# Optimization experiments

Hardware: AMD Instinct MI355X
Metric: run time of the kernel (lower is better)

Reference implementation:

```python
import jax, jax.numpy as jnp
import numpy as np

B, S, H, I = 2, 2048, 1024, 2816
NUM_EXPERTS = 8
NUM_SHARED = 1
E_ROUTED = NUM_EXPERTS - NUM_SHARED  # 7
TOP_K = 2


def setup_inputs() -> dict:
    key = jax.random.key(0)
    ks = jax.random.split(key, 9)
    scale = 0.02
    return {
        "x": jax.random.normal(ks[0], (B, S, H), jnp.float32),
        "router_w": jax.random.normal(ks[1], (H, E_ROUTED), jnp.float32) * scale,
        "routing_bias": jnp.zeros((E_ROUTED,), jnp.float32),
        "shared_gate": jax.random.normal(ks[2], (H, I), jnp.float32) * scale,
        "shared_up": jax.random.normal(ks[3], (H, I), jnp.float32) * scale,
        "shared_down": jax.random.normal(ks[4], (I, H), jnp.float32) * scale,
        "routed_gate": jax.random.normal(ks[5], (E_ROUTED, H, I), jnp.float32) * scale,
        "routed_up": jax.random.normal(ks[6], (E_ROUTED, H, I), jnp.float32) * scale,
        "routed_down": jax.random.normal(ks[7], (E_ROUTED, I, H), jnp.float32) * scale,
    }


def _mlp(x, gate_w, up_w, down_w):
    # SwiGLU MLP: down( silu(x@gate) * (x@up) )
    return (jax.nn.silu(x @ gate_w) * (x @ up_w)) @ down_w


def reference(x, router_w, routing_bias, shared_gate, shared_up, shared_down,
              routed_gate, routed_up, routed_down):
    e_routed = routed_gate.shape[0]
    # shared expert path (num_shared_experts == 1, no averaging)
    shared_out = _mlp(x, shared_gate, shared_up, shared_down)  # [B,S,H]

    # sigmoid router with bias, top-k, renormalize
    routing_logits = x @ router_w + routing_bias           # [B,S,E]
    routing_probs = jax.nn.sigmoid(routing_logits)
    scores, indices = jax.lax.top_k(routing_probs, TOP_K)  # [B,S,K]
    scores = scores / scores.sum(axis=-1, keepdims=True)

    # per-token combine weight for each expert: sum over top-k slots
    onehot = jax.nn.one_hot(indices, e_routed, dtype=x.dtype)   # [B,S,K,E]
    combine = jnp.einsum("bsk,bske->bse", scores, onehot)       # [B,S,E]

    out = shared_out
    for e in range(e_routed):  # fixed small expert count
        expert_out = _mlp(x, routed_gate[e], routed_up[e], routed_down[e])
        out = out + combine[..., e:e + 1] * expert_out
    return out
```

## Files before the change

### kernel.cpp

```cpp
#include <hip/hip_runtime.h>
#include <hip/hip_bf16.h>

#define TT 4096
#define HD 1024
#define ID 2816
#define ER 7
#define HI (HD * ID)

typedef short s16x8 __attribute__((ext_vector_type(8)));
typedef float f32x4 __attribute__((ext_vector_type(4)));

__device__ __forceinline__ uint32_t pkbf(float a, float b) {
    union { __hip_bfloat16 h[2]; uint32_t u; } z;
    z.h[0] = __float2bfloat16(a);
    z.h[1] = __float2bfloat16(b);
    return z.u;
}

__device__ __forceinline__ void gl_lds16(const void* g, void* l) {
    __builtin_amdgcn_global_load_lds(
        (const __attribute__((address_space(1))) uint32_t*)g,
        (__attribute__((address_space(3))) uint32_t*)l, 16, 0, 0);
}

__global__ __launch_bounds__(64) void router_kernel(
    const float* __restrict__ x, const float* __restrict__ rw,
    const float* __restrict__ rbias, float* __restrict__ combine)
{
    const int t = blockIdx.x;
    const int lane = threadIdx.x;
    const float* xt = x + (size_t)t * HD;
    float acc[ER];
#pragma unroll
    for (int e = 0; e < ER; ++e) acc[e] = 0.f;
    for (int h = lane; h < HD; h += 64) {
        const float xv = xt[h];
#pragma unroll
        for (int e = 0; e < ER; ++e)
            acc[e] += xv * rw[h * ER + e];
    }
#pragma unroll
    for (int e = 0; e < ER; ++e) {
        float v = acc[e];
#pragma unroll
        for (int off = 32; off > 0; off >>= 1) v += __shfl_down(v, off, 64);
        acc[e] = v;
    }
    if (lane == 0) {
        float p[ER];
#pragma unroll
        for (int e = 0; e < ER; ++e) {
            const float lg = acc[e] + rbias[e];
            p[e] = 1.f / (1.f + __expf(-lg));
        }
        int i1 = 0;
#pragma unroll
        for (int e = 1; e < ER; ++e) if (p[e] > p[i1]) i1 = e;
        int i2 = (i1 == 0) ? 1 : 0;
#pragma unroll
        for (int e = 0; e < ER; ++e) {
            if (e == i1 || e == i2) continue;
            if (p[e] > p[i2]) i2 = e;
        }
        const float s = p[i1] + p[i2];
        float w[8];
#pragma unroll
        for (int e = 0; e < 8; ++e) w[e] = 0.f;
        w[i1] = p[i1] / s;
        w[i2] = p[i2] / s;
        w[7] = 1.f;
        float* cb = combine + (size_t)t * 8;
#pragma unroll
        for (int e = 0; e < 8; ++e) cb[e] = w[e];
    }
}

__global__ __launch_bounds__(256) void txp_kernel(
    const float* __restrict__ Wsh, const float* __restrict__ Wrt,
    __hip_bfloat16* __restrict__ dst, int K, int N)
{
    __shared__ float lds[64 * 65];
    const int z = blockIdx.z;
    const float* src = (z < ER) ? (Wrt + (size_t)z * HI) : Wsh;
    __hip_bfloat16* out = dst + (size_t)z * HI;
    const int n0 = blockIdx.x * 64, k0 = blockIdx.y * 64;
    const int t = threadIdx.x;
    const int r = t >> 4, c = (t & 15) * 4;
#pragma unroll
    for (int i = 0; i < 4; ++i) {
        const float4 v = *(const float4*)(src + (size_t)(k0 + r + 16 * i) * N + n0 + c);
        float* p = &lds[(r + 16 * i) * 65 + c];
        p[0] = v.x; p[1] = v.y; p[2] = v.z; p[3] = v.w;
    }
    __syncthreads();
    const int nr = t >> 3, kc = (t & 7) * 8;
#pragma unroll
    for (int i = 0; i < 2; ++i) {
        const int nn = nr + 32 * i;
        uint32_t w[4];
#pragma unroll
        for (int j = 0; j < 4; ++j)
            w[j] = pkbf(lds[(kc + 2 * j) * 65 + nn], lds[(kc + 2 * j + 1) * 65 + nn]);
        *(uint4*)(out + (size_t)(n0 + nn) * K + k0 + kc) = *(uint4*)w;
    }
}

__global__ __launch_bounds__(256) void cvt_kernel(
    const float* __restrict__ a, __hip_bfloat16* __restrict__ o)
{
    const size_t i = ((size_t)blockIdx.x * 256 + threadIdx.x) * 8;
    const float4 v0 = *(const float4*)(a + i);
    const float4 v1 = *(const float4*)(a + i + 4);
    uint32_t w[4] = { pkbf(v0.x, v0.y), pkbf(v0.z, v0.w),
                      pkbf(v1.x, v1.y), pkbf(v1.z, v1.w) };
    *(uint4*)(o + i) = *(uint4*)w;
}

__global__ __launch_bounds__(256) void zero_kernel(float* __restrict__ o)
{
    const size_t i = ((size_t)blockIdx.x * 256 + threadIdx.x) * 4;
    *(float4*)(o + i) = float4{0.f, 0.f, 0.f, 0.f};
}

__global__ __launch_bounds__(256) void gu_kernel_g(
    const __hip_bfloat16* __restrict__ X,
    const __hip_bfloat16* __restrict__ Wg,
    const __hip_bfloat16* __restrict__ Wu,
    const float* __restrict__ combine,
    __hip_bfloat16* __restrict__ H,
    int e0)
{
    __shared__ __hip_bfloat16 sA[128 * 32];
    __shared__ __hip_bfloat16 sG[128 * 32];
    __shared__ __hip_bfloat16 sU[128 * 32];
    const int tid = threadIdx.x;
    const int g = gridDim.z;

    const int lid = blockIdx.x + 22 * blockIdx.y + 704 * blockIdx.z;
    const int xcd = lid & 7;
    const int w = lid >> 3;
    const int xpe = 8 / g;
    const int el = xcd / xpe;
    const int t = xcd % xpe;
    const int cx = (xpe >= 2) ? 2 : 1;
    const int tw = 22 / cx;
    const int th = 32 / (xpe / cx);
    const int bx = (t % cx) * tw + (w % tw);
    const int by = (t / cx) * th + (w / tw);

    const int e = e0 + el;
    const int n0 = bx * 128, m0 = by * 128;
    const __hip_bfloat16* Bg = Wg + (size_t)e * HI;
    const __hip_bfloat16* Bu = Wu + (size_t)e * HI;
    const int ldH = g * ID;

    const int lane = tid & 63, wave = tid >> 6;
    const int wm = (wave >> 1) * 64, wn = (wave & 1) * 64;
    const int r = lane & 15, quad = lane >> 4;

    f32x4 ag[4][4], au[4][4];
#pragma unroll
    for (int i = 0; i < 4; ++i)
#pragma unroll
        for (int j = 0; j < 4; ++j) {
            ag[i][j] = (f32x4){0.f, 0.f, 0.f, 0.f};
            au[i][j] = (f32x4){0.f, 0.f, 0.f, 0.f};
        }

    const int srow = tid >> 2;
    const int sk = ((tid & 3) ^ ((srow >> 1) & 3)) * 8;
    const size_t aoff = (size_t)(m0 + srow) * HD + sk;
    const size_t boff = (size_t)(n0 + srow) * HD + sk;
    char* lA = (char*)sA + tid * 16;
    char* lG = (char*)sG + tid * 16;
    char* lU = (char*)sU + tid * 16;

    const int xh = ((quad ^ ((r >> 1) & 3)) << 4);

    for (int kb = 0; kb < HD; kb += 32) {
        gl_lds16(X + aoff + kb, lA);
        gl_lds16(X + aoff + (size_t)64 * HD + kb, lA + 4096);
        gl_lds16(Bg + boff + kb, lG);
        gl_lds16(Bg + boff + (size_t)64 * HD + kb, lG + 4096);
        gl_lds16(Bu + boff + kb, lU);
        gl_lds16(Bu + boff + (size_t)64 * HD + kb, lU + 4096);
        __syncthreads();

        s16x8 af[4], bg[4], bu[4];
#pragma unroll
        for (int mi = 0; mi < 4; ++mi)
            af[mi] = *(const s16x8*)((const char*)sA + (wm + mi * 16 + r) * 64 + xh);
#pragma unroll
        for (int ni = 0; ni < 4; ++ni) {
            bg[ni] = *(const s16x8*)((const char*)sG + (wn + ni * 16 + r) * 64 + xh);
            bu[ni] = *(const s16x8*)((const char*)sU + (wn + ni * 16 + r) * 64 + xh);
        }
#pragma unroll
        for (int mi = 0; mi < 4; ++mi)
#pragma unroll
            for (int ni = 0; ni < 4; ++ni) {
                ag[mi][ni] = __builtin_amdgcn_mfma_f32_16x16x32_bf16(af[mi], bg[ni], ag[mi][ni], 0, 0, 0);
                au[mi][ni] = __builtin_amdgcn_mfma_f32_16x16x32_bf16(af[mi], bu[ni], au[mi][ni], 0, 0, 0);
            }
        __syncthreads();
    }

    const int colb = el * ID;
#pragma unroll
    for (int mi = 0; mi < 4; ++mi)
#pragma unroll
        for (int i = 0; i < 4; ++i) {
            const int grow = m0 + wm + mi * 16 + quad * 4 + i;
            const float wcb = combine[(size_t)grow * 8 + e];
#pragma unroll
            for (int ni = 0; ni < 4; ++ni) {
                const int gcol = n0 + wn + ni * 16 + r;
                const float gv = ag[mi][ni][i];
                const float uv = au[mi][ni][i];
                const float hv = (gv / (1.f + __expf(-gv))) * uv * wcb;
                H[(size_t)grow * ldH + colb + gcol] = __float2bfloat16(hv);
            }
        }
}

__global__ __launch_bounds__(256) void down_kernel_g(
    const __hip_bfloat16* __restrict__ Hb,
    const __hip_bfloat16* __restrict__ Wd,
    float* __restrict__ Out, int g)
{
    __shared__ __hip_bfloat16 sA[128 * 32];
    __shared__ __hip_bfloat16 sB[128 * 32];
    const int tid = threadIdx.x;

    const int lid = blockIdx.x + 8 * blockIdx.y + 256 * blockIdx.z;
    const int xcd = lid & 7;
    const int w = lid >> 3;
    const int sz = xcd >> 2;
    const int q = xcd & 3;
    const int bx = (q & 1) * 4 + (w & 3);
    const int by = (q >> 1) * 16 + (w >> 2);

    const int n0 = bx * 128, m0 = by * 128;
    const int ldH = g * ID;
    int e_b, e_e, k0, k1;
    if (g == 1) { e_b = 0; e_e = 1; k0 = sz * (ID / 2); k1 = k0 + ID / 2; }
    else        { e_b = sz * (g >> 1); e_e = e_b + (g >> 1); k0 = 0; k1 = ID; }

    const int lane = tid & 63, wave = tid >> 6;
    const int wm = (wave >> 1) * 64, wn = (wave & 1) * 64;
    const int r = lane & 15, quad = lane >> 4;

    f32x4 acc[4][4];
#pragma unroll
    for (int i = 0; i < 4; ++i)
#pragma unroll
        for (int j = 0; j < 4; ++j)
            acc[i][j] = (f32x4){0.f, 0.f, 0.f, 0.f};

    const int srow = tid >> 2;
    const int sk = ((tid & 3) ^ ((srow >> 1) & 3)) * 8;
    char* lA = (char*)sA + tid * 16;
    char* lB = (char*)sB + tid * 16;
    const int xh = ((quad ^ ((r >> 1) & 3)) << 4);

    for (int e = e_b; e < e_e; ++e) {
        const size_t abase = (size_t)(m0 + srow) * ldH + (size_t)e * ID + sk;
        const size_t bbase = (size_t)e * HI + (size_t)(n0 + srow) * ID + sk;
        for (int kb = k0; kb < k1; kb += 32) {
            gl_lds16(Hb + abase + kb, lA);
            gl_lds16(Hb + abase + (size_t)64 * ldH + kb, lA + 4096);
            gl_lds16(Wd + bbase + kb, lB);
            gl_lds16(Wd + bbase + (size_t)64 * ID + kb, lB + 4096);
            __syncthreads();

            s16x8 af[4], bf[4];
#pragma unroll
            for (int mi = 0; mi < 4; ++mi)
                af[mi] = *(const s16x8*)((const char*)sA + (wm + mi * 16 + r) * 64 + xh);
#pragma unroll
            for (int ni = 0; ni < 4; ++ni)
                bf[ni] = *(const s16x8*)((const char*)sB + (wn + ni * 16 + r) * 64 + xh);
#pragma unroll
            for (int mi = 0; mi < 4; ++mi)
#pragma unroll
                for (int ni = 0; ni < 4; ++ni)
                    acc[mi][ni] = __builtin_amdgcn_mfma_f32_16x16x32_bf16(af[mi], bf[ni], acc[mi][ni], 0, 0, 0);
            __syncthreads();
        }
    }

#pragma unroll
    for (int mi = 0; mi < 4; ++mi)
#pragma unroll
        for (int i = 0; i < 4; ++i) {
            const int grow = m0 + wm + mi * 16 + quad * 4 + i;
#pragma unroll
            for (int ni = 0; ni < 4; ++ni) {
                const int gcol = n0 + wn + ni * 16 + r;
                atomicAdd(&Out[(size_t)grow * HD + gcol], acc[mi][ni][i]);
            }
        }
}

template <int MODE, int AF32>
__global__ __launch_bounds__(256) void gemm_kernel(
    const void* __restrict__ Av, const float* __restrict__ B,
    __hip_bfloat16* __restrict__ Hbuf, float* __restrict__ Out,
    const float* __restrict__ combine, int M, int N, int K, int wcol, int beta)
{
    __shared__ uint32_t ldsA[128 * 20];
    __shared__ uint32_t ldsB[128 * 20];
    const int tid = threadIdx.x;
    const int n0 = blockIdx.x * 128;
    const int m0 = blockIdx.y * 128;
    const int lane = tid & 63, wave = tid >> 6;
    const int wm = (wave >> 1) * 64, wn = (wave & 1) * 64;
    const int r = lane & 15, quad = lane >> 4;
    f32x4 acc[4][4];
#pragma unroll
    for (int i = 0; i < 4; ++i)
#pragma unroll
        for (int j = 0; j < 4; ++j) acc[i][j] = (f32x4){0.f, 0.f, 0.f, 0.f};
    for (int kb = 0; kb < K; kb += 32) {
        if (AF32) {
            const float* A = (const float*)Av;
            const int arow = tid >> 1, ah = tid & 1;
            const float* ap = A + (size_t)(m0 + arow) * K + kb + ah * 16;
            const float4 f0 = *(const float4*)ap;
            const float4 f1 = *(const float4*)(ap + 4);
            const float4 f2 = *(const float4*)(ap + 8);
            const float4 f3 = *(const float4*)(ap + 12);
            uint4 w0, w1;
            w0.x = pkbf(f0.x, f0.y); w0.y = pkbf(f0.z, f0.w);
            w0.z = pkbf(f1.x, f1.y); w0.w = pkbf(f1.z, f1.w);
            w1.x = pkbf(f2.x, f2.y); w1.y = pkbf(f2.z, f2.w);
            w1.z = pkbf(f3.x, f3.y); w1.w = pkbf(f3.z, f3.w);
            *(uint4*)&ldsA[arow * 20 + ah * 8] = w0;
            *(uint4*)&ldsA[arow * 20 + ah * 8 + 4] = w1;
        } else {
            const __hip_bfloat16* A = (const __hip_bfloat16*)Av;
            const int arow = tid >> 2, akc = tid & 3;
            const uint4 v0 = *(const uint4*)(A + (size_t)(m0 + arow) * K + kb + akc * 8);
            const uint4 v1 = *(const uint4*)(A + (size_t)(m0 + arow + 64) * K + kb + akc * 8);
            *(uint4*)&ldsA[arow * 20 + akc * 4] = v0;
            *(uint4*)&ldsA[(arow + 64) * 20 + akc * 4] = v1;
        }
        {
            const int bkp = tid >> 4, bnc = tid & 15;
            const float* bp0 = B + (size_t)(kb + 2 * bkp) * N + n0 + bnc * 8;
            const float* bp1 = bp0 + N;
            const float4 a0 = *(const float4*)bp0;
            const float4 a1 = *(const float4*)(bp0 + 4);
            const float4 b0 = *(const float4*)bp1;
            const float4 b1 = *(const float4*)(bp1 + 4);
            const float r0[8] = {a0.x, a0.y, a0.z, a0.w, a1.x, a1.y, a1.z, a1.w};
            const float r1[8] = {b0.x, b0.y, b0.z, b0.w, b1.x, b1.y, b1.z, b1.w};
            const int grp = (((bkp >> 2) ^ (bnc & 3)) << 2);
            const int kk = bkp & 3;
#pragma unroll
            for (int j = 0; j < 8; ++j)
                ldsB[(bnc * 8 + j) * 20 + grp + kk] = pkbf(r0[j], r1[j]);
        }
        __syncthreads();
        s16x8 af[4], bfr[4];
#pragma unroll
        for (int mi = 0; mi < 4; ++mi)
            af[mi] = *(const s16x8*)&ldsA[(wm + mi * 16 + r) * 20 + quad * 4];
#pragma unroll
        for (int ni = 0; ni < 4; ++ni) {
            const int nl = wn + ni * 16 + r;
            bfr[ni] = *(const s16x8*)&ldsB[nl * 20 + ((quad ^ ((nl >> 3) & 3)) << 2)];
        }
#pragma unroll
        for (int mi = 0; mi < 4; ++mi)
#pragma unroll
            for (int ni = 0; ni < 4; ++ni)
                acc[mi][ni] = __builtin_amdgcn_mfma_f32_16x16x32_bf16(af[mi], bfr[ni], acc[mi][ni], 0, 0, 0);
        __syncthreads();
    }
#pragma unroll
    for (int mi = 0; mi < 4; ++mi)
#pragma unroll
        for (int i = 0; i < 4; ++i) {
            const int grow = m0 + wm + mi * 16 + quad * 4 + i;
#pragma unroll
            for (int ni = 0; ni < 4; ++ni) {
                const int gcol = n0 + wn + ni * 16 + r;
                const float v = acc[mi][ni][i];
                if (MODE == 0) {
                    Hbuf[(size_t)grow * N + gcol] = __float2bfloat16(v / (1.f + __expf(-v)));
                } else if (MODE == 1) {
                    const size_t idx = (size_t)grow * N + gcol;
                    Hbuf[idx] = __float2bfloat16(__bfloat162float(Hbuf[idx]) * v);
                } else {
                    const size_t idx = (size_t)grow * N + gcol;
                    const float w = combine[(size_t)grow * 8 + wcol];
                    Out[idx] = (beta ? Out[idx] : 0.f) + w * v;
                }
            }
        }
}

extern "C" void kernel_launch(void* const* d_in, const int* in_sizes, int n_in,
                              void* d_out, int out_size, void* d_ws, size_t ws_size,
                              hipStream_t stream)
{
    (void)in_sizes; (void)n_in; (void)out_size;
    const float* x  = (const float*)d_in[0];
    const float* rw = (const float*)d_in[1];
    const float* rb = (const float*)d_in[2];
    const float* sg = (const float*)d_in[3];
    const float* su = (const float*)d_in[4];
    const float* sd = (const float*)d_in[5];
    const float* rg = (const float*)d_in[6];
    const float* ru = (const float*)d_in[7];
    const float* rd = (const float*)d_in[8];
    float* out = (float*)d_out;

    const size_t SZ_COMBINE = (size_t)TT * 8 * 4;
    const size_t SZ_XB      = (size_t)TT * HD * 2;
    const size_t SZ_W       = (size_t)8 * HI * 2;

    int g = 0;
    for (int c = 8; c >= 1; c >>= 1) {
        const size_t need = SZ_COMBINE + SZ_XB + (size_t)TT * c * ID * 2 + 3 * SZ_W;
        if (ws_size >= need) { g = c; break; }
    }

    if (g) {
        char* p = (char*)d_ws;
        float* combine = (float*)p;            p += SZ_COMBINE;
        __hip_bfloat16* xb   = (__hip_bfloat16*)p; p += SZ_XB;
        __hip_bfloat16* hbuf = (__hip_bfloat16*)p; p += (size_t)TT * g * ID * 2;
        __hip_bfloat16* wtg  = (__hip_bfloat16*)p; p += SZ_W;
        __hip_bfloat16* wtu  = (__hip_bfloat16*)p; p += SZ_W;
        __hip_bfloat16* wtd  = (__hip_bfloat16*)p;

        zero_kernel<<<(TT * HD) / 1024, 256, 0, stream>>>(out);
        cvt_kernel<<<(TT * HD) / 2048, 256, 0, stream>>>(x, xb);
        txp_kernel<<<dim3(ID / 64, HD / 64, 8), 256, 0, stream>>>(sg, rg, wtg, HD, ID);
        txp_kernel<<<dim3(ID / 64, HD / 64, 8), 256, 0, stream>>>(su, ru, wtu, HD, ID);
        txp_kernel<<<dim3(HD / 64, ID / 64, 8), 256, 0, stream>>>(sd, rd, wtd, ID, HD);
        router_kernel<<<TT, 64, 0, stream>>>(x, rw, rb, combine);

        for (int gi = 0; gi < 8 / g; ++gi) {
            gu_kernel_g<<<dim3(22, 32, g), 256, 0, stream>>>(
                xb, wtg, wtu, combine, hbuf, gi * g);
            down_kernel_g<<<dim3(8, 32, 2), 256, 0, stream>>>(
                hbuf, wtd + (size_t)gi * g * HI, out, g);
        }
    } else {
        float* combine = (float*)d_ws;
        __hip_bfloat16* hbuf = (__hip_bfloat16*)(combine + (size_t)TT * 8);
        router_kernel<<<TT, 64, 0, stream>>>(x, rw, rb, combine);
        dim3 blk(256);
        dim3 gH(ID / 128, TT / 128);
        dim3 gD(HD / 128, TT / 128);
        for (int p = 0; p < 8; ++p) {
            const float *wg, *wu, *wd;
            if (p < ER) {
                wg = rg + (size_t)p * HI;
                wu = ru + (size_t)p * HI;
                wd = rd + (size_t)p * HI;
            } else {
                wg = sg; wu = su; wd = sd;
            }
            gemm_kernel<0, 1><<<gH, blk, 0, stream>>>(x, wg, hbuf, nullptr, nullptr, TT, ID, HD, 0, 0);
            gemm_kernel<1, 1><<<gH, blk, 0, stream>>>(x, wu, hbuf, nullptr, nullptr, TT, ID, HD, 0, 0);
            gemm_kernel<2, 0><<<gD, blk, 0, stream>>>(hbuf, wd, nullptr, out, combine, TT, HD, ID, p, p == 0 ? 0 : 1);
        }
    }
}
```

Baseline: 1.358 ms.

## Double-buffer LDS tiles in gate/up and down GEMM kernels

Adds two LDS buffers per operand so the global-to-LDS load of the next K slice is issued before the MFMAs on the current slice. The goal is to hide global load latency behind compute, replacing the previous load, sync, compute, sync sequence. LDS use doubles (48KB for gate/up), which can lower occupancy. The loop assumes an even number of 32-wide K steps; HD/32=32 and ID/2/32=44 both satisfy this.

Measured after the change: 1.295 ms. 4.7% less time.

```diff
diff --git a/kernel.cpp b/kernel.cpp
--- a/kernel.cpp
+++ b/kernel.cpp
@@ -122,6 +122,45 @@
     *(float4*)(o + i) = float4{0.f, 0.f, 0.f, 0.f};
 }
 
+__device__ __forceinline__ void gu_stage(
+    const __hip_bfloat16* __restrict__ X,
+    const __hip_bfloat16* __restrict__ Bg,
+    const __hip_bfloat16* __restrict__ Bu,
+    size_t aoff, size_t boff, int kb, char* lA, char* lG, char* lU)
+{
+    gl_lds16(X + aoff + kb, lA);
+    gl_lds16(X + aoff + (size_t)64 * HD + kb, lA + 4096);
+    gl_lds16(Bg + boff + kb, lG);
+    gl_lds16(Bg + boff + (size_t)64 * HD + kb, lG + 4096);
+    gl_lds16(Bu + boff + kb, lU);
+    gl_lds16(Bu + boff + (size_t)64 * HD + kb, lU + 4096);
+}
+
+__device__ __forceinline__ void gu_mma(
+    const __hip_bfloat16* __restrict__ sA,
+    const __hip_bfloat16* __restrict__ sG,
+    const __hip_bfloat16* __restrict__ sU,
+    int wm, int wn, int r, int xh,
+    f32x4 (&ag)[4][4], f32x4 (&au)[4][4])
+{
+    s16x8 af[4], bg[4], bu[4];
+#pragma unroll
+    for (int mi = 0; mi < 4; ++mi)
+        af[mi] = *(const s16x8*)((const char*)sA + (wm + mi * 16 + r) * 64 + xh);
+#pragma unroll
+    for (int ni = 0; ni < 4; ++ni) {
+        bg[ni] = *(const s16x8*)((const char*)sG + (wn + ni * 16 + r) * 64 + xh);
+        bu[ni] = *(const s16x8*)((const char*)sU + (wn + ni * 16 + r) * 64 + xh);
+    }
+#pragma unroll
+    for (int mi = 0; mi < 4; ++mi)
+#pragma unroll
+        for (int ni = 0; ni < 4; ++ni) {
+            ag[mi][ni] = __builtin_amdgcn_mfma_f32_16x16x32_bf16(af[mi], bg[ni], ag[mi][ni], 0, 0, 0);
+            au[mi][ni] = __builtin_amdgcn_mfma_f32_16x16x32_bf16(af[mi], bu[ni], au[mi][ni], 0, 0, 0);
+        }
+}
+
 __global__ __launch_bounds__(256) void gu_kernel_g(
     const __hip_bfloat16* __restrict__ X,
     const __hip_bfloat16* __restrict__ Wg,
@@ -130,9 +169,9 @@
     __hip_bfloat16* __restrict__ H,
     int e0)
 {
-    __shared__ __hip_bfloat16 sA[128 * 32];
-    __shared__ __hip_bfloat16 sG[128 * 32];
-    __shared__ __hip_bfloat16 sU[128 * 32];
+    __shared__ __hip_bfloat16 sA[2][128 * 32];
+    __shared__ __hip_bfloat16 sG[2][128 * 32];
+    __shared__ __hip_bfloat16 sU[2][128 * 32];
     const int tid = threadIdx.x;
     const int g = gridDim.z;
 
@@ -171,37 +210,26 @@
     const int sk = ((tid & 3) ^ ((srow >> 1) & 3)) * 8;
     const size_t aoff = (size_t)(m0 + srow) * HD + sk;
     const size_t boff = (size_t)(n0 + srow) * HD + sk;
-    char* lA = (char*)sA + tid * 16;
-    char* lG = (char*)sG + tid * 16;
-    char* lU = (char*)sU + tid * 16;
+    char* lA0 = (char*)&sA[0][0] + tid * 16;
+    char* lG0 = (char*)&sG[0][0] + tid * 16;
+    char* lU0 = (char*)&sU[0][0] + tid * 16;
+    char* lA1 = (char*)&sA[1][0] + tid * 16;
+    char* lG1 = (char*)&sG[1][0] + tid * 16;
+    char* lU1 = (char*)&sU[1][0] + tid * 16;
 
     const int xh = ((quad ^ ((r >> 1) & 3)) << 4);
 
-    for (int kb = 0; kb < HD; kb += 32) {
-        gl_lds16(X + aoff + kb, lA);
-        gl_lds16(X + aoff + (size_t)64 * HD + kb, lA + 4096);
-        gl_lds16(Bg + boff + kb, lG);
-        gl_lds16(Bg + boff + (size_t)64 * HD + kb, lG + 4096);
-        gl_lds16(Bu + boff + kb, lU);
-        gl_lds16(Bu + boff + (size_t)64 * HD + kb, lU + 4096);
+    gu_stage(X, Bg, Bu, aoff, boff, 0, lA0, lG0, lU0);
+    __syncthreads();
+
+    for (int kb = 0; kb < HD; kb += 64) {
+        if (kb + 32 < HD)
+            gu_stage(X, Bg, Bu, aoff, boff, kb + 32, lA1, lG1, lU1);
+        gu_mma(&sA[0][0], &sG[0][0], &sU[0][0], wm, wn, r, xh, ag, au);
         __syncthreads();
-
-        s16x8 af[4], bg[4], bu[4];
-#pragma unroll
-        for (int mi = 0; mi < 4; ++mi)
-            af[mi] = *(const s16x8*)((const char*)sA + (wm + mi * 16 + r) * 64 + xh);
-#pragma unroll
-        for (int ni = 0; ni < 4; ++ni) {
-            bg[ni] = *(const s16x8*)((const char*)sG + (wn + ni * 16 + r) * 64 + xh);
-            bu[ni] = *(const s16x8*)((const char*)sU + (wn + ni * 16 + r) * 64 + xh);
-        }
-#pragma unroll
-        for (int mi = 0; mi < 4; ++mi)
-#pragma unroll
-            for (int ni = 0; ni < 4; ++ni) {
-                ag[mi][ni] = __builtin_amdgcn_mfma_f32_16x16x32_bf16(af[mi], bg[ni], ag[mi][ni], 0, 0, 0);
-                au[mi][ni] = __builtin_amdgcn_mfma_f32_16x16x32_bf16(af[mi], bu[ni], au[mi][ni], 0, 0, 0);
-            }
+        if (kb + 64 < HD)
+            gu_stage(X, Bg, Bu, aoff, boff, kb + 64, lA0, lG0, lU0);
+        gu_mma(&sA[1][0], &sG[1][0], &sU[1][0], wm, wn, r, xh, ag, au);
         __syncthreads();
     }
 
@@ -223,13 +251,43 @@
         }
 }
 
+__device__ __forceinline__ void dn_stage(
+    const __hip_bfloat16* __restrict__ Hb,
+    const __hip_bfloat16* __restrict__ Wd,
+    size_t abase, size_t bbase, int ldH, int kb, char* lA, char* lB)
+{
+    gl_lds16(Hb + abase + kb, lA);
+    gl_lds16(Hb + abase + (size_t)64 * ldH + kb, lA + 4096);
+    gl_lds16(Wd + bbase + kb, lB);
+    gl_lds16(Wd + bbase + (size_t)64 * ID + kb, lB + 4096);
+}
+
+__device__ __forceinline__ void dn_mma(
+    const __hip_bfloat16* __restrict__ sA,
+    const __hip_bfloat16* __restrict__ sB,
+    int wm, int wn, int r, int xh, f32x4 (&acc)[4][4])
+{
+    s16x8 af[4], bf[4];
+#pragma unroll
+    for (int mi = 0; mi < 4; ++mi)
+        af[mi] = *(const s16x8*)((const char*)sA + (wm + mi * 16 + r) * 64 + xh);
+#pragma unroll
+    for (int ni = 0; ni < 4; ++ni)
+        bf[ni] = *(const s16x8*)((const char*)sB + (wn + ni * 16 + r) * 64 + xh);
+#pragma unroll
+    for (int mi = 0; mi < 4; ++mi)
+#pragma unroll
+        for (int ni = 0; ni < 4; ++ni)
+            acc[mi][ni] = __builtin_amdgcn_mfma_f32_16x16x32_bf16(af[mi], bf[ni], acc[mi][ni], 0, 0, 0);
+}
+
 __global__ __launch_bounds__(256) void down_kernel_g(
     const __hip_bfloat16* __restrict__ Hb,
     const __hip_bfloat16* __restrict__ Wd,
     float* __restrict__ Out, int g)
 {
-    __shared__ __hip_bfloat16 sA[128 * 32];
-    __shared__ __hip_bfloat16 sB[128 * 32];
+    __shared__ __hip_bfloat16 sA[2][128 * 32];
+    __shared__ __hip_bfloat16 sB[2][128 * 32];
     const int tid = threadIdx.x;
 
     const int lid = blockIdx.x + 8 * blockIdx.y + 256 * blockIdx.z;
@@ -259,32 +317,26 @@
 
     const int srow = tid >> 2;
     const int sk = ((tid & 3) ^ ((srow >> 1) & 3)) * 8;
-    char* lA = (char*)sA + tid * 16;
-    char* lB = (char*)sB + tid * 16;
+    char* lA0 = (char*)&sA[0][0] + tid * 16;
+    char* lB0 = (char*)&sB[0][0] + tid * 16;
+    char* lA1 = (char*)&sA[1][0] + tid * 16;
+    char* lB1 = (char*)&sB[1][0] + tid * 16;
     const int xh = ((quad ^ ((r >> 1) & 3)) << 4);
 
     for (int e = e_b; e < e_e; ++e) {
         const size_t abase = (size_t)(m0 + srow) * ldH + (size_t)e * ID + sk;
         const size_t bbase = (size_t)e * HI + (size_t)(n0 + srow) * ID + sk;
-        for (int kb = k0; kb < k1; kb += 32) {
-            gl_lds16(Hb + abase + kb, lA);
-            gl_lds16(Hb + abase + (size_t)64 * ldH + kb, lA + 4096);
-            gl_lds16(Wd + bbase + kb, lB);
-            gl_lds16(Wd + bbase + (size_t)64 * ID + kb, lB + 4096);
+
+        dn_stage(Hb, Wd, abase, bbase, ldH, k0, lA0, lB0);
+        __syncthreads();
+        for (int kb = k0; kb < k1; kb += 64) {
+            if (kb + 32 < k1)
+                dn_stage(Hb, Wd, abase, bbase, ldH, kb + 32, lA1, lB1);
+            dn_mma(&sA[0][0], &sB[0][0], wm, wn, r, xh, acc);
             __syncthreads();
-
-            s16x8 af[4], bf[4];
-#pragma unroll
-            for (int mi = 0; mi < 4; ++mi)
-                af[mi] = *(const s16x8*)((const char*)sA + (wm + mi * 16 + r) * 64 + xh);
-#pragma unroll
-            for (int ni = 0; ni < 4; ++ni)
-                bf[ni] = *(const s16x8*)((const char*)sB + (wn + ni * 16 + r) * 64 + xh);
-#pragma unroll
-            for (int mi = 0; mi < 4; ++mi)
-#pragma unroll
-                for (int ni = 0; ni < 4; ++ni)
-                    acc[mi][ni] = __builtin_amdgcn_mfma_f32_16x16x32_bf16(af[mi], bf[ni], acc[mi][ni], 0, 0, 0);
+            if (kb + 64 < k1)
+                dn_stage(Hb, Wd, abase, bbase, ldH, kb + 64, lA0, lB0);
+            dn_mma(&sA[1][0], &sB[1][0], wm, wn, r, xh, acc);
             __syncthreads();
         }
     }
```

## Triple-buffer LDS tiles with async prefetch in gate-up and down GEMMs

Applied to the files above, without the earlier changes.

Replaces the load-sync-compute-sync loop in both expert GEMM kernels with a three-stage LDS ring. Tiles are prefetched two steps ahead via global_load_lds, with explicit vmcnt waits and a single barrier per iteration. This lets global memory latency overlap with MFMA work and removes one barrier per k-step. In exchange, LDS use per block triples (to 72KB for gate-up), which may lower occupancy, and correctness now depends on the hand-counted vmcnt values.

New measurement: 1.405 ms. 3.5% more time.

```diff
diff --git a/kernel.cpp b/kernel.cpp
--- a/kernel.cpp
+++ b/kernel.cpp
@@ -22,6 +22,13 @@
         (const __attribute__((address_space(1))) uint32_t*)g,
         (__attribute__((address_space(3))) uint32_t*)l, 16, 0, 0);
 }
+
+#define WAITV6 asm volatile("s_waitcnt vmcnt(6)" ::: "memory")
+#define WAITV4 asm volatile("s_waitcnt vmcnt(4)" ::: "memory")
+#define WAITV0 asm volatile("s_waitcnt vmcnt(0)" ::: "memory")
+#define SBAR do { __builtin_amdgcn_sched_barrier(0); \
+                  __builtin_amdgcn_s_barrier();      \
+                  __builtin_amdgcn_sched_barrier(0); } while (0)
 
 __global__ __launch_bounds__(64) void router_kernel(
     const float* __restrict__ x, const float* __restrict__ rw,
@@ -122,6 +129,29 @@
     *(float4*)(o + i) = float4{0.f, 0.f, 0.f, 0.f};
 }
 
+__device__ __forceinline__ void gu_mma(
+    const char* bA, const char* bG, const char* bU,
+    int wm, int wn, int r, int xh,
+    f32x4 (&ag)[4][4], f32x4 (&au)[4][4])
+{
+    s16x8 af[4], bg[4], bu[4];
+#pragma unroll
+    for (int mi = 0; mi < 4; ++mi)
+        af[mi] = *(const s16x8*)(bA + (wm + mi * 16 + r) * 64 + xh);
+#pragma unroll
+    for (int ni = 0; ni < 4; ++ni) {
+        bg[ni] = *(const s16x8*)(bG + (wn + ni * 16 + r) * 64 + xh);
+        bu[ni] = *(const s16x8*)(bU + (wn + ni * 16 + r) * 64 + xh);
+    }
+#pragma unroll
+    for (int mi = 0; mi < 4; ++mi)
+#pragma unroll
+        for (int ni = 0; ni < 4; ++ni) {
+            ag[mi][ni] = __builtin_amdgcn_mfma_f32_16x16x32_bf16(af[mi], bg[ni], ag[mi][ni], 0, 0, 0);
+            au[mi][ni] = __builtin_amdgcn_mfma_f32_16x16x32_bf16(af[mi], bu[ni], au[mi][ni], 0, 0, 0);
+        }
+}
+
 __global__ __launch_bounds__(256) void gu_kernel_g(
     const __hip_bfloat16* __restrict__ X,
     const __hip_bfloat16* __restrict__ Wg,
@@ -130,9 +160,9 @@
     __hip_bfloat16* __restrict__ H,
     int e0)
 {
-    __shared__ __hip_bfloat16 sA[128 * 32];
-    __shared__ __hip_bfloat16 sG[128 * 32];
-    __shared__ __hip_bfloat16 sU[128 * 32];
+    __shared__ __hip_bfloat16 sA[3][128 * 32];
+    __shared__ __hip_bfloat16 sG[3][128 * 32];
+    __shared__ __hip_bfloat16 sU[3][128 * 32];
     const int tid = threadIdx.x;
     const int g = gridDim.z;
 
@@ -171,39 +201,40 @@
     const int sk = ((tid & 3) ^ ((srow >> 1) & 3)) * 8;
     const size_t aoff = (size_t)(m0 + srow) * HD + sk;
     const size_t boff = (size_t)(n0 + srow) * HD + sk;
-    char* lA = (char*)sA + tid * 16;
-    char* lG = (char*)sG + tid * 16;
-    char* lU = (char*)sU + tid * 16;
 
     const int xh = ((quad ^ ((r >> 1) & 3)) << 4);
 
-    for (int kb = 0; kb < HD; kb += 32) {
-        gl_lds16(X + aoff + kb, lA);
-        gl_lds16(X + aoff + (size_t)64 * HD + kb, lA + 4096);
-        gl_lds16(Bg + boff + kb, lG);
-        gl_lds16(Bg + boff + (size_t)64 * HD + kb, lG + 4096);
-        gl_lds16(Bu + boff + kb, lU);
-        gl_lds16(Bu + boff + (size_t)64 * HD + kb, lU + 4096);
-        __syncthreads();
-
-        s16x8 af[4], bg[4], bu[4];
-#pragma unroll
-        for (int mi = 0; mi < 4; ++mi)
-            af[mi] = *(const s16x8*)((const char*)sA + (wm + mi * 16 + r) * 64 + xh);
-#pragma unroll
-        for (int ni = 0; ni < 4; ++ni) {
-            bg[ni] = *(const s16x8*)((const char*)sG + (wn + ni * 16 + r) * 64 + xh);
-            bu[ni] = *(const s16x8*)((const char*)sU + (wn + ni * 16 + r) * 64 + xh);
-        }
-#pragma unroll
-        for (int mi = 0; mi < 4; ++mi)
-#pragma unroll
-            for (int ni = 0; ni < 4; ++ni) {
-                ag[mi][ni] = __builtin_amdgcn_mfma_f32_16x16x32_bf16(af[mi], bg[ni], ag[mi][ni], 0, 0, 0);
-                au[mi][ni] = __builtin_amdgcn_mfma_f32_16x16x32_bf16(af[mi], bu[ni], au[mi][ni], 0, 0, 0);
-            }
-        __syncthreads();
-    }
+#define GU_STAGE(kb, bo) do {                                            \
+        char* dA = (char*)sA + (bo) + tid * 16;                          \
+        char* dG = (char*)sG + (bo) + tid * 16;                          \
+        char* dU = (char*)sU + (bo) + tid * 16;                          \
+        gl_lds16(X + aoff + (kb), dA);                                   \
+        gl_lds16(X + aoff + (size_t)64 * HD + (kb), dA + 4096);          \
+        gl_lds16(Bg + boff + (kb), dG);                                  \
+        gl_lds16(Bg + boff + (size_t)64 * HD + (kb), dG + 4096);         \
+        gl_lds16(Bu + boff + (kb), dU);                                  \
+        gl_lds16(Bu + boff + (size_t)64 * HD + (kb), dU + 4096);         \
+    } while (0)
+
+    const int nt = HD / 32;
+    GU_STAGE(0, 0);
+    GU_STAGE(32, 8192);
+    unsigned boR = 0, boS = 16384;
+
+    for (int tt = 0; tt < nt - 1; ++tt) {
+        WAITV6;
+        SBAR;
+        if (tt + 2 < nt) GU_STAGE((tt + 2) * 32, boS);
+        gu_mma((const char*)sA + boR, (const char*)sG + boR,
+               (const char*)sU + boR, wm, wn, r, xh, ag, au);
+        boR = (boR == 16384u) ? 0u : boR + 8192u;
+        boS = (boS == 16384u) ? 0u : boS + 8192u;
+    }
+    WAITV0;
+    SBAR;
+    gu_mma((const char*)sA + boR, (const char*)sG + boR,
+           (const char*)sU + boR, wm, wn, r, xh, ag, au);
+#undef GU_STAGE
 
     const int colb = el * ID;
 #pragma unroll
@@ -223,13 +254,31 @@
         }
 }
 
+__device__ __forceinline__ void dn_mma(
+    const char* bA, const char* bB,
+    int wm, int wn, int r, int xh, f32x4 (&acc)[4][4])
+{
+    s16x8 af[4], bf[4];
+#pragma unroll
+    for (int mi = 0; mi < 4; ++mi)
+        af[mi] = *(const s16x8*)(bA + (wm + mi * 16 + r) * 64 + xh);
+#pragma unroll
+    for (int ni = 0; ni < 4; ++ni)
+        bf[ni] = *(const s16x8*)(bB + (wn + ni * 16 + r) * 64 + xh);
+#pragma unroll
+    for (int mi = 0; mi < 4; ++mi)
+#pragma unroll
+        for (int ni = 0; ni < 4; ++ni)
+            acc[mi][ni] = __builtin_amdgcn_mfma_f32_16x16x32_bf16(af[mi], bf[ni], acc[mi][ni], 0, 0, 0);
+}
+
 __global__ __launch_bounds__(256) void down_kernel_g(
     const __hip_bfloat16* __restrict__ Hb,
     const __hip_bfloat16* __restrict__ Wd,
     float* __restrict__ Out, int g)
 {
-    __shared__ __hip_bfloat16 sA[128 * 32];
-    __shared__ __hip_bfloat16 sB[128 * 32];
+    __shared__ __hip_bfloat16 sA[3][128 * 32];
+    __shared__ __hip_bfloat16 sB[3][128 * 32];
     const int tid = threadIdx.x;
 
     const int lid = blockIdx.x + 8 * blockIdx.y + 256 * blockIdx.z;
@@ -259,35 +308,42 @@
 
     const int srow = tid >> 2;
     const int sk = ((tid & 3) ^ ((srow >> 1) & 3)) * 8;
-    char* lA = (char*)sA + tid * 16;
-    char* lB = (char*)sB + tid * 16;
     const int xh = ((quad ^ ((r >> 1) & 3)) << 4);
+
+#define DN_STAGE(kb, bo) do {                                            \
+        char* dA = (char*)sA + (bo) + tid * 16;                          \
+        char* dB = (char*)sB + (bo) + tid * 16;                          \
+        gl_lds16(Hb + abase + (kb), dA);                                 \
+        gl_lds16(Hb + abase + (size_t)64 * ldH + (kb), dA + 4096);       \
+        gl_lds16(Wd + bbase + (kb), dB);                                 \
+        gl_lds16(Wd + bbase + (size_t)64 * ID + (kb), dB + 4096);        \
+    } while (0)
 
     for (int e = e_b; e < e_e; ++e) {
         const size_t abase = (size_t)(m0 + srow) * ldH + (size_t)e * ID + sk;
         const size_t bbase = (size_t)e * HI + (size_t)(n0 + srow) * ID + sk;
-        for (int kb = k0; kb < k1; kb += 32) {
-            gl_lds16(Hb + abase + kb, lA);
-            gl_lds16(Hb + abase + (size_t)64 * ldH + kb, lA + 4096);
-            gl_lds16(Wd + bbase + kb, lB);
-            gl_lds16(Wd + bbase + (size_t)64 * ID + kb, lB + 4096);
-            __syncthreads();
-
-            s16x8 af[4], bf[4];
-#pragma unroll
-            for (int mi = 0; mi < 4; ++mi)
-                af[mi] = *(const s16x8*)((const char*)sA + (wm + mi * 16 + r) * 64 + xh);
-#pragma unroll
-            for (int ni = 0; ni < 4; ++ni)
-                bf[ni] = *(const s16x8*)((const char*)sB + (wn + ni * 16 + r) * 64 + xh);
-#pragma unroll
-            for (int mi = 0; mi < 4; ++mi)
-#pragma unroll
-                for (int ni = 0; ni < 4; ++ni)
-                    acc[mi][ni] = __builtin_amdgcn_mfma_f32_16x16x32_bf16(af[mi], bf[ni], acc[mi][ni], 0, 0, 0);
-            __syncthreads();
-        }
-    }
+        const int nt = (k1 - k0) / 32;
+
+        DN_STAGE(k0, 0);
+        DN_STAGE(k0 + 32, 8192);
+        unsigned boR = 0, boS = 16384;
+
+        for (int tt = 0; tt < nt - 1; ++tt) {
+            WAITV4;
+            SBAR;
+            if (tt + 2 < nt) DN_STAGE(k0 + (tt + 2) * 32, boS);
+            dn_mma((const char*)sA + boR, (const char*)sB + boR,
+                   wm, wn, r, xh, acc);
+            boR = (boR == 16384u) ? 0u : boR + 8192u;
+            boS = (boS == 16384u) ? 0u : boS + 8192u;
+        }
+        WAITV0;
+        SBAR;
+        dn_mma((const char*)sA + boR, (const char*)sB + boR,
+               wm, wn, r, xh, acc);
+        if (e + 1 < e_e) SBAR;
+    }
+#undef DN_STAGE
 
 #pragma unroll
     for (int mi = 0; mi < 4; ++mi)
```
